# Kernel optimization log

Measured on AMD Instinct MI355X. Metric: run time of the kernel, lower is better.

Reference implementation:

```python
import jax, jax.numpy as jnp
import numpy as np

N_HEADS = 24
ROPE_BASE = 10000.0


def apply_rope(x, offset):
    """x: (B, H, L, Dh). Rotate pairs per RoPE (Su et al., 2021)."""
    B, H, L, Dh = x.shape
    inv_freq = 1.0 / (ROPE_BASE ** (jnp.arange(0, Dh, 2, dtype=jnp.float32) / Dh))  # (Dh/2,)
    t = jnp.arange(L, dtype=jnp.float32) + offset                                   # (L,)
    freqs = jnp.outer(t, inv_freq)                                                  # (L, Dh/2)
    emb = jnp.concatenate([freqs, freqs], axis=-1)                                  # (L, Dh)
    cos = jnp.cos(emb).astype(x.dtype)
    sin = jnp.sin(emb).astype(x.dtype)
    x1, x2 = x[..., : Dh // 2], x[..., Dh // 2 :]
    rotated = jnp.concatenate([-x2, x1], axis=-1)
    return x * cos + rotated * sin


def setup_inputs() -> dict:
    key = jax.random.key(0)
    k1, k2, k3 = jax.random.split(key, 3)
    B, L, D = 4, 2048, 1536
    x = jax.random.normal(k1, (B, L, D), dtype=jnp.float32)
    # Linear weights, torch convention (out_features, in_features), scaled init
    w_qkv = jax.random.normal(k2, (3 * D, D), dtype=jnp.float32) * 0.02
    w_out = jax.random.normal(k3, (D, D), dtype=jnp.float32) * 0.02
    return {"x": x, "w_qkv": w_qkv, "w_out": w_out, "pos_offset": 0}


def reference(x, w_qkv, w_out, pos_offset):
    B, L, D = x.shape
    H = N_HEADS
    Dh = D // H
    # fused QKV projection (no bias)
    qkv = jnp.einsum('bld,ed->ble', x, w_qkv)              # (B, L, 3D)
    qkv = qkv.reshape(B, L, 3, H, Dh)
    q = qkv[:, :, 0].transpose(0, 2, 1, 3)                 # (B, H, L, Dh)
    k = qkv[:, :, 1].transpose(0, 2, 1, 3)
    v = qkv[:, :, 2].transpose(0, 2, 1, 3)
    q = apply_rope(q, pos_offset)
    k = apply_rope(k, pos_offset)
    scale = 1.0 / np.sqrt(Dh)
    scores = jnp.einsum('bhqd,bhkd->bhqk', q, k) * scale   # (B, H, L, L)
    causal = jnp.tril(jnp.ones((L, L), dtype=bool))
    scores = jnp.where(causal, scores, jnp.finfo(scores.dtype).min)
    attn = jax.nn.softmax(scores, axis=-1)
    out = jnp.einsum('bhqk,bhkd->bhqd', attn, v)           # (B, H, L, Dh)
    out = out.transpose(0, 2, 1, 3).reshape(B, L, D)
    return jnp.einsum('bld,ed->ble', out, w_out)           # (B, L, D)
```

## Files before the change

kernel.cpp:

```cpp
#include <hip/hip_runtime.h>
#include <hip/hip_bf16.h>
#include <math.h>

typedef unsigned short u16;
typedef __bf16 b8 __attribute__((ext_vector_type(8)));
typedef __bf16 bf2t __attribute__((ext_vector_type(2)));
typedef float f4 __attribute__((ext_vector_type(4)));

#define B_ 4
#define L_ 2048
#define D_ 1536
#define H_ 24
#define DH_ 64

__device__ __forceinline__ float bf2f(u16 v) {
    union { unsigned u; float f; } z; z.u = ((unsigned)v) << 16; return z.f;
}
__device__ __forceinline__ u16 f2bf(float f) {
    union { float f; unsigned u; } z; z.f = f;
    unsigned u = z.u;
    return (u16)((u + 0x7fffu + ((u >> 16) & 1u)) >> 16);
}
__device__ __forceinline__ void f4_to_bf4(f4 v, u16 o[4]) {
#if __has_builtin(__builtin_amdgcn_cvt_pk_bf16_f32)
    union { bf2t b; unsigned u; } z0, z1;
    z0.b = __builtin_amdgcn_cvt_pk_bf16_f32(v[0], v[1]);
    z1.b = __builtin_amdgcn_cvt_pk_bf16_f32(v[2], v[3]);
    o[0] = (u16)(z0.u & 0xffffu); o[1] = (u16)(z0.u >> 16);
    o[2] = (u16)(z1.u & 0xffffu); o[3] = (u16)(z1.u >> 16);
#else
    o[0] = f2bf(v[0]); o[1] = f2bf(v[1]); o[2] = f2bf(v[2]); o[3] = f2bf(v[3]);
#endif
}

__global__ __launch_bounds__(256) void cvt_f32_bf16(const float* __restrict__ src,
                                                    u16* __restrict__ dst, int n4) {
    int i = blockIdx.x * 256 + threadIdx.x;
    if (i >= n4) return;
    float4 vv = ((const float4*)src)[i];
    f4 v = {vv.x, vv.y, vv.z, vv.w};
    u16 o4[4];
    f4_to_bf4(v, o4);
    ushort4 o = {o4[0], o4[1], o4[2], o4[3]};
    ((ushort4*)dst)[i] = o;
}

__global__ __launch_bounds__(256) void gemm128(const u16* __restrict__ A,
                                               const u16* __restrict__ B,
                                               float* __restrict__ Cf,
                                               u16* __restrict__ Qp,
                                               u16* __restrict__ Kp,
                                               u16* __restrict__ Vp,
                                               int M, int N, int K, int mode) {
    __shared__ u16 As[128 * 32];
    __shared__ u16 Bs[128 * 32];
    const int tid = threadIdx.x;
    const int wave = tid >> 6, lane = tid & 63;
    const int m16 = lane & 15, quad = lane >> 4;
    const int bm = blockIdx.y * 128, bn = blockIdx.x * 128;
    const int wr = (wave >> 1) * 64, wc = (wave & 1) * 64;

    f4 acc[4][4];
#pragma unroll
    for (int i = 0; i < 4; i++)
#pragma unroll
        for (int j = 0; j < 4; j++) acc[i][j] = (f4)0.0f;

    const int c0 = wave * 64 + lane;
    const int r0 = c0 >> 2, col0 = (c0 & 3) * 8;
    const int c1 = c0 + 256;
    const int r1 = c1 >> 2, col1 = (c1 & 3) * 8;

    for (int k0 = 0; k0 < K; k0 += 32) {
        __syncthreads();
        __builtin_amdgcn_global_load_lds(
            (const __attribute__((address_space(1))) void*)(A + (size_t)(bm + r0) * K + k0 + col0),
            (__attribute__((address_space(3))) void*)(As + (size_t)c0 * 8), 16, 0, 0);
        __builtin_amdgcn_global_load_lds(
            (const __attribute__((address_space(1))) void*)(A + (size_t)(bm + r1) * K + k0 + col1),
            (__attribute__((address_space(3))) void*)(As + (size_t)c1 * 8), 16, 0, 0);
        __builtin_amdgcn_global_load_lds(
            (const __attribute__((address_space(1))) void*)(B + (size_t)(bn + r0) * K + k0 + col0),
            (__attribute__((address_space(3))) void*)(Bs + (size_t)c0 * 8), 16, 0, 0);
        __builtin_amdgcn_global_load_lds(
            (const __attribute__((address_space(1))) void*)(B + (size_t)(bn + r1) * K + k0 + col1),
            (__attribute__((address_space(3))) void*)(Bs + (size_t)c1 * 8), 16, 0, 0);
        __syncthreads();
        b8 af[4], bfm[4];
#pragma unroll
        for (int i = 0; i < 4; i++) af[i] = *(const b8*)(As + (wr + i * 16 + m16) * 32 + quad * 8);
#pragma unroll
        for (int j = 0; j < 4; j++) bfm[j] = *(const b8*)(Bs + (wc + j * 16 + m16) * 32 + quad * 8);
#pragma unroll
        for (int i = 0; i < 4; i++)
#pragma unroll
            for (int j = 0; j < 4; j++)
                acc[i][j] = __builtin_amdgcn_mfma_f32_16x16x32_bf16(af[i], bfm[j], acc[i][j], 0, 0, 0);
    }

    if (mode == 0) {
#pragma unroll
        for (int i = 0; i < 4; i++)
#pragma unroll
            for (int j = 0; j < 4; j++)
#pragma unroll
                for (int r = 0; r < 4; r++) {
                    int row = bm + wr + i * 16 + quad * 4 + r;
                    int col = bn + wc + j * 16 + m16;
                    Cf[(size_t)row * N + col] = acc[i][j][r];
                }
    } else {
#pragma unroll
        for (int j = 0; j < 4; j++) {
            const int colbase = bn + wc + j * 16;
            const int s = colbase / D_;
            const int h = (colbase % D_) / DH_;
            const int dh0 = colbase % DH_;
            u16* dst = (s == 0) ? Qp : ((s == 1) ? Kp : Vp);
#pragma unroll
            for (int i = 0; i < 4; i++) {
                u16 o4[4];
                f4_to_bf4(acc[i][j], o4);
#pragma unroll
                for (int r = 0; r < 4; r++) {
                    int row = bm + wr + i * 16 + quad * 4 + r;
                    int b = row >> 11, l = row & (L_ - 1);
                    dst[((size_t)(b * H_ + h) * L_ + l) * DH_ + dh0 + m16] = o4[r];
                }
            }
        }
    }
}

__global__ __launch_bounds__(256) void rope_inplace(u16* __restrict__ Qp,
                                                    u16* __restrict__ Kp,
                                                    const int* __restrict__ pos) {
    unsigned idx = blockIdx.x * 256 + threadIdx.x;
    int i = idx & 31;
    unsigned t1 = idx >> 5;
    int l = t1 & (L_ - 1);
    unsigned t2 = t1 >> 11;
    int h = t2 % H_;
    int b = t2 / H_;
    float t = (float)(l + pos[0]);
    float invf = powf(10000.0f, -(float)(2 * i) * (1.0f / 64.0f));
    float ang = t * invf;
    float c = cosf(ang), s = sinf(ang);
    size_t base = ((size_t)(b * H_ + h) * L_ + l) * DH_;
    {
        float x1 = bf2f(Qp[base + i]), x2 = bf2f(Qp[base + i + 32]);
        Qp[base + i] = f2bf((x1 * c - x2 * s) * 0.125f);
        Qp[base + i + 32] = f2bf((x2 * c + x1 * s) * 0.125f);
    }
    {
        float x1 = bf2f(Kp[base + i]), x2 = bf2f(Kp[base + i + 32]);
        Kp[base + i] = f2bf(x1 * c - x2 * s);
        Kp[base + i + 32] = f2bf(x2 * c + x1 * s);
    }
}

__global__ __launch_bounds__(256, 3) void attn(const u16* __restrict__ Q,
                                               const u16* __restrict__ K,
                                               const u16* __restrict__ V,
                                               u16* __restrict__ O) {
    __shared__ u16 Ks[64 * 72];
    __shared__ u16 Vs[64 * 72];
    __shared__ u16 Ps[4][32 * 72];
    const int tid = threadIdx.x;
    const int wave = tid >> 6, lane = tid & 63;
    const int m16 = lane & 15, quad = lane >> 4;
    const int bh = blockIdx.y;
    const int tA = blockIdx.x;
    const int tB = 15 - tA;
    const int qA = tA * 128 + wave * 32;
    const int qB = tB * 128 + wave * 32;
    const int srow = tid >> 2, scol = (tid & 3) * 16, g = (tid & 3);

    b8 qfA[2][2], qfB[2][2];
#pragma unroll
    for (int i = 0; i < 2; i++) {
        const u16* qa = Q + ((size_t)bh * L_ + qA + i * 16 + m16) * DH_;
        qfA[i][0] = *(const b8*)(qa + quad * 8);
        qfA[i][1] = *(const b8*)(qa + 32 + quad * 8);
        const u16* qb = Q + ((size_t)bh * L_ + qB + i * 16 + m16) * DH_;
        qfB[i][0] = *(const b8*)(qb + quad * 8);
        qfB[i][1] = *(const b8*)(qb + 32 + quad * 8);
    }

    float lrA[2][4], lrB[2][4];
    f4 oaccA[2][4], oaccB[2][4];
#pragma unroll
    for (int i = 0; i < 2; i++)
#pragma unroll
        for (int r = 0; r < 4; r++) { lrA[i][r] = 0.0f; lrB[i][r] = 0.0f; }
#pragma unroll
    for (int i = 0; i < 2; i++)
#pragma unroll
        for (int n = 0; n < 4; n++) { oaccA[i][n] = (f4)0.0f; oaccB[i][n] = (f4)0.0f; }

    u16* pw = Ps[wave];

    auto process = [&](int qw, b8 (&qf)[2][2], float (&lrow)[2][4], f4 (&oacc)[2][4],
                       int kbase) {
        const bool need_mask = (kbase + 64 > qw);
        f4 s[2][4];
#pragma unroll
        for (int sub = 0; sub < 4; sub++) {
            b8 k0 = *(const b8*)(Ks + (sub * 16 + m16) * 72 + quad * 8);
            b8 k1 = *(const b8*)(Ks + (sub * 16 + m16) * 72 + 32 + quad * 8);
#pragma unroll
            for (int i = 0; i < 2; i++) {
                f4 c = (f4)0.0f;
                c = __builtin_amdgcn_mfma_f32_16x16x32_bf16(qf[i][0], k0, c, 0, 0, 0);
                c = __builtin_amdgcn_mfma_f32_16x16x32_bf16(qf[i][1], k1, c, 0, 0, 0);
                s[i][sub] = c;
            }
        }
        if (need_mask) {
#pragma unroll
            for (int i = 0; i < 2; i++)
#pragma unroll
                for (int sub = 0; sub < 4; sub++)
#pragma unroll
                    for (int r = 0; r < 4; r++) {
                        const int key = kbase + sub * 16 + m16;
                        const int qg = qw + i * 16 + quad * 4 + r;
                        float p = __expf(s[i][sub][r]);
                        p = (key <= qg) ? p : 0.0f;
                        s[i][sub][r] = p;
                        lrow[i][r] += p;
                    }
        } else {
#pragma unroll
            for (int i = 0; i < 2; i++)
#pragma unroll
                for (int sub = 0; sub < 4; sub++)
#pragma unroll
                    for (int r = 0; r < 4; r++) {
                        float p = __expf(s[i][sub][r]);
                        s[i][sub][r] = p;
                        lrow[i][r] += p;
                    }
        }
#pragma unroll
        for (int i = 0; i < 2; i++)
#pragma unroll
            for (int sub = 0; sub < 4; sub++) {
                u16 o4[4];
                f4_to_bf4(s[i][sub], o4);
#pragma unroll
                for (int r = 0; r < 4; r++)
                    pw[(i * 16 + quad * 4 + r) * 72 + sub * 16 + m16] = o4[r];
            }
#pragma unroll
        for (int ks = 0; ks < 2; ks++) {
            b8 pf[2];
#pragma unroll
            for (int i = 0; i < 2; i++)
                pf[i] = *(const b8*)(pw + (i * 16 + m16) * 72 + ks * 32 + quad * 8);
#pragma unroll
            for (int n = 0; n < 4; n++) {
                b8 vf = *(const b8*)(Vs + (n * 16 + m16) * 72 +
                                     ((ks * 32 + quad * 8 + n * 16) & 63));
#pragma unroll
                for (int i = 0; i < 2; i++)
                    oacc[i][n] = __builtin_amdgcn_mfma_f32_16x16x32_bf16(pf[i], vf, oacc[i][n], 0, 0, 0);
            }
        }
    };

    const int nkt = 2 * tB + 2;
    for (int kt = 0; kt < nkt; kt++) {
        const int kbase = kt * 64;
        __syncthreads();
        {
            const u16* kg = K + ((size_t)bh * L_ + kbase + srow) * DH_ + scol;
            uint4 a0 = *(const uint4*)kg;
            uint4 a1 = *(const uint4*)(kg + 8);
            const u16* vg = V + ((size_t)bh * L_ + kbase + srow) * DH_ + scol;
            uint4 b0 = *(const uint4*)vg;
            uint4 b1 = *(const uint4*)(vg + 8);
            *(uint4*)(Ks + srow * 72 + scol) = a0;
            *(uint4*)(Ks + srow * 72 + scol + 8) = a1;
            u16 tmp[16];
            *(uint4*)(tmp) = b0;
            *(uint4*)(tmp + 8) = b1;
#pragma unroll
            for (int e = 0; e < 16; e++)
                Vs[(scol + e) * 72 + ((srow + g * 16) & 63)] = tmp[e];
        }
        __syncthreads();
        if (kbase <= qA + 31) process(qA, qfA, lrA, oaccA, kbase);
        if (kbase <= qB + 31) process(qB, qfB, lrB, oaccB, kbase);
    }

#pragma unroll
    for (int x = 1; x < 16; x <<= 1)
#pragma unroll
        for (int i = 0; i < 2; i++)
#pragma unroll
            for (int r = 0; r < 4; r++) {
                lrA[i][r] += __shfl_xor(lrA[i][r], x, 64);
                lrB[i][r] += __shfl_xor(lrB[i][r], x, 64);
            }
    const int b = bh / H_, h = bh % H_;
#pragma unroll
    for (int i = 0; i < 2; i++)
#pragma unroll
        for (int r = 0; r < 4; r++) {
            const float invA = 1.0f / lrA[i][r];
            const float invB = 1.0f / lrB[i][r];
            const int qa = qA + i * 16 + quad * 4 + r;
            const int qb = qB + i * 16 + quad * 4 + r;
#pragma unroll
            for (int n = 0; n < 4; n++) {
                O[((size_t)(b * L_ + qa)) * D_ + h * 64 + n * 16 + m16] = f2bf(oaccA[i][n][r] * invA);
                O[((size_t)(b * L_ + qb)) * D_ + h * 64 + n * 16 + m16] = f2bf(oaccB[i][n][r] * invB);
            }
        }
}

extern "C" void kernel_launch(void* const* d_in, const int* in_sizes, int n_in,
                              void* d_out, int out_size, void* d_ws, size_t ws_size,
                              hipStream_t stream) {
    const float* x = (const float*)d_in[0];
    const float* w_qkv = (const float*)d_in[1];
    const float* w_out = (const float*)d_in[2];
    const int* pos = (const int*)d_in[3];
    float* out = (float*)d_out;

    const size_t nx = (size_t)B_ * L_ * D_;
    const size_t nwq = (size_t)3 * D_ * D_;
    const size_t nwo = (size_t)D_ * D_;
    const size_t per = (size_t)B_ * H_ * L_ * DH_;

    u16* xb = (u16*)d_ws;
    u16* wqkvb = xb + nx;
    u16* woutb = wqkvb + nwq;
    u16* Qp = woutb + nwo;
    u16* Kp = Qp + per;
    u16* Vp = Kp + per;
    u16* aO = xb;

    cvt_f32_bf16<<<(int)((nx / 4 + 255) / 256), 256, 0, stream>>>(x, xb, (int)(nx / 4));
    cvt_f32_bf16<<<(int)((nwq / 4 + 255) / 256), 256, 0, stream>>>(w_qkv, wqkvb, (int)(nwq / 4));
    cvt_f32_bf16<<<(int)((nwo / 4 + 255) / 256), 256, 0, stream>>>(w_out, woutb, (int)(nwo / 4));

    gemm128<<<dim3(3 * D_ / 128, B_ * L_ / 128), 256, 0, stream>>>(
        xb, wqkvb, nullptr, Qp, Kp, Vp, B_ * L_, 3 * D_, D_, 1);
    rope_inplace<<<(B_ * H_ * L_ * 32) / 256, 256, 0, stream>>>(Qp, Kp, pos);
    attn<<<dim3(L_ / 256, B_ * H_), 256, 0, stream>>>(Qp, Kp, Vp, aO);
    gemm128<<<dim3(D_ / 128, B_ * L_ / 128), 256, 0, stream>>>(
        aO, woutb, out, nullptr, nullptr, nullptr, B_ * L_, D_, D_, 0);
}
```

Measured before the change: 522.9 us.

## Replace 128x128 GEMM with double-buffered 256x256 ping-pong pipelined GEMM

Swaps the simple 128x128 tile GEMM, which has one barrier-separated load and compute phase per K=32 step, for a 256x256 tile kernel with 512 threads. It double-buffers K=64 slabs in 128KB of LDS with an XOR-swizzled layout and streams global-to-LDS loads in halves, interleaved with MFMA phases using s_setprio and explicit vmcnt waits. The goal is to hide memory latency behind MFMA work and raise data reuse in both projection GEMMs. The cost is many more barriers, heavy register use, and a smaller grid (e.g. 6x32 blocks for the output projection), which may underfill the CUs.

After: 503.6 us. 3.7% less time.

```diff
diff --git a/kernel.cpp b/kernel.cpp
--- a/kernel.cpp
+++ b/kernel.cpp
@@ -45,87 +45,192 @@
     ((ushort4*)dst)[i] = o;
 }
 
-__global__ __launch_bounds__(256) void gemm128(const u16* __restrict__ A,
-                                               const u16* __restrict__ B,
-                                               float* __restrict__ Cf,
-                                               u16* __restrict__ Qp,
-                                               u16* __restrict__ Kp,
-                                               u16* __restrict__ Vp,
-                                               int M, int N, int K, int mode) {
-    __shared__ u16 As[128 * 32];
-    __shared__ u16 Bs[128 * 32];
+
+__device__ __forceinline__ void stage_half(const u16* __restrict__ G, int Kd,
+                                           int row0, int k0, char* region, int tid) {
+#pragma unroll
+    for (int q = 0; q < 2; q++) {
+        const int p = (q * 512 + tid) * 16;
+        const int l = p ^ (((p >> 9) & 1) << 5);
+        const int grow = row0 + (l >> 11) * 16 + ((l >> 6) & 15);
+        const int gcol = k0 + (((((l >> 10) & 1) << 6) + (l & 63)) >> 1);
+        __builtin_amdgcn_global_load_lds(
+            (const __attribute__((address_space(1))) void*)(G + (size_t)grow * Kd + gcol),
+            (__attribute__((address_space(3))) void*)(region + p), 16, 0, 0);
+    }
+}
+
+template <int BUF, int MH>
+__device__ __forceinline__ void lda(const char* ldsb, int wm, int lo, b8 (&aR)[4][2]) {
+#pragma unroll
+    for (int i = 0; i < 4; i++)
+#pragma unroll
+        for (int ks = 0; ks < 2; ks++)
+            aR[i][ks] = *(const b8*)(ldsb + BUF * 32768 + wm * 16384 +
+                                     ((MH * 4 + i) * 2 + ks) * 1024 + lo);
+}
+template <int BUF, int NH>
+__device__ __forceinline__ void ldb(const char* ldsb, int wn, int lo, b8 (&bR)[4][2]) {
+#pragma unroll
+    for (int j = 0; j < 2; j++)
+#pragma unroll
+        for (int ks = 0; ks < 2; ks++)
+            bR[NH * 2 + j][ks] = *(const b8*)(ldsb + 65536 + BUF * 32768 + (wn >> 1) * 16384 +
+                                              (((wn & 1) * 4 + NH * 2 + j) * 2 + ks) * 1024 + lo);
+}
+template <int MH, int NH>
+__device__ __forceinline__ void mfma16(b8 (&aR)[4][2], b8 (&bR)[4][2], f4 (&acc)[8][4]) {
+    __builtin_amdgcn_s_setprio(1);
+#pragma unroll
+    for (int ks = 0; ks < 2; ks++)
+#pragma unroll
+        for (int i = 0; i < 4; i++)
+#pragma unroll
+            for (int j = 0; j < 2; j++)
+                acc[MH * 4 + i][NH * 2 + j] = __builtin_amdgcn_mfma_f32_16x16x32_bf16(
+                    aR[i][ks], bR[NH * 2 + j][ks], acc[MH * 4 + i][NH * 2 + j], 0, 0, 0);
+    __builtin_amdgcn_s_setprio(0);
+}
+
+__global__ __launch_bounds__(512, 2) void gemm256(const u16* __restrict__ A,
+                                                  const u16* __restrict__ B,
+                                                  float* __restrict__ Cf,
+                                                  u16* __restrict__ Qp,
+                                                  u16* __restrict__ Kp,
+                                                  u16* __restrict__ Vp,
+                                                  int M, int N, int K, int mode) {
+    __shared__ uint4 ldsv[131072 / 16];
+    char* ldsb = (char*)ldsv;
     const int tid = threadIdx.x;
     const int wave = tid >> 6, lane = tid & 63;
     const int m16 = lane & 15, quad = lane >> 4;
-    const int bm = blockIdx.y * 128, bn = blockIdx.x * 128;
-    const int wr = (wave >> 1) * 64, wc = (wave & 1) * 64;
-
-    f4 acc[4][4];
-#pragma unroll
-    for (int i = 0; i < 4; i++)
+    const int wm = wave >> 2, wn = wave & 3;
+    const int bm = blockIdx.y * 256, bn = blockIdx.x * 256;
+    int lo = m16 * 64 + quad * 16;
+    lo ^= (m16 & 8) << 2;
+
+    char* const As0 = ldsb;
+    char* const As1 = ldsb + 32768;
+    char* const Bs0 = ldsb + 65536;
+    char* const Bs1 = ldsb + 98304;
+
+    f4 acc[8][4];
+#pragma unroll
+    for (int i = 0; i < 8; i++)
 #pragma unroll
         for (int j = 0; j < 4; j++) acc[i][j] = (f4)0.0f;
 
-    const int c0 = wave * 64 + lane;
-    const int r0 = c0 >> 2, col0 = (c0 & 3) * 8;
-    const int c1 = c0 + 256;
-    const int r1 = c1 >> 2, col1 = (c1 & 3) * 8;
-
-    for (int k0 = 0; k0 < K; k0 += 32) {
-        __syncthreads();
-        __builtin_amdgcn_global_load_lds(
-            (const __attribute__((address_space(1))) void*)(A + (size_t)(bm + r0) * K + k0 + col0),
-            (__attribute__((address_space(3))) void*)(As + (size_t)c0 * 8), 16, 0, 0);
-        __builtin_amdgcn_global_load_lds(
-            (const __attribute__((address_space(1))) void*)(A + (size_t)(bm + r1) * K + k0 + col1),
-            (__attribute__((address_space(3))) void*)(As + (size_t)c1 * 8), 16, 0, 0);
-        __builtin_amdgcn_global_load_lds(
-            (const __attribute__((address_space(1))) void*)(B + (size_t)(bn + r0) * K + k0 + col0),
-            (__attribute__((address_space(3))) void*)(Bs + (size_t)c0 * 8), 16, 0, 0);
-        __builtin_amdgcn_global_load_lds(
-            (const __attribute__((address_space(1))) void*)(B + (size_t)(bn + r1) * K + k0 + col1),
-            (__attribute__((address_space(3))) void*)(Bs + (size_t)c1 * 8), 16, 0, 0);
-        __syncthreads();
-        b8 af[4], bfm[4];
-#pragma unroll
-        for (int i = 0; i < 4; i++) af[i] = *(const b8*)(As + (wr + i * 16 + m16) * 32 + quad * 8);
-#pragma unroll
-        for (int j = 0; j < 4; j++) bfm[j] = *(const b8*)(Bs + (wc + j * 16 + m16) * 32 + quad * 8);
-#pragma unroll
-        for (int i = 0; i < 4; i++)
-#pragma unroll
-            for (int j = 0; j < 4; j++)
-                acc[i][j] = __builtin_amdgcn_mfma_f32_16x16x32_bf16(af[i], bfm[j], acc[i][j], 0, 0, 0);
+    b8 aR[4][2], bR[4][2];
+
+    stage_half(A, K, bm, 0, As0, tid);
+    stage_half(A, K, bm + 128, 0, As0 + 16384, tid);
+    stage_half(B, K, bn, 0, Bs0, tid);
+    stage_half(B, K, bn + 128, 0, Bs0 + 16384, tid);
+    stage_half(B, K, bn, 64, Bs1, tid);
+    stage_half(A, K, bm, 64, As1, tid);
+    asm volatile("s_waitcnt vmcnt(4)" ::: "memory");
+    __builtin_amdgcn_s_barrier();
+    __builtin_amdgcn_sched_barrier(0);
+
+    const int NIT = K >> 7;
+#pragma unroll 1
+    for (int it = 0; it < NIT; ++it) {
+        const bool more = (it + 1 < NIT);
+        const int k1 = (2 * it + 1) << 6;
+        const int k2 = (2 * it + 2) << 6;
+        const int k3 = (2 * it + 3) << 6;
+
+        lda<0, 0>(ldsb, wm, lo, aR);
+        ldb<0, 0>(ldsb, wn, lo, bR);
+        stage_half(A, K, bm + 128, k1, As1 + 16384, tid);
+        __builtin_amdgcn_s_barrier();
+        mfma16<0, 0>(aR, bR, acc);
+        __builtin_amdgcn_s_barrier();
+
+        ldb<0, 1>(ldsb, wn, lo, bR);
+        stage_half(B, K, bn + 128, k1, Bs1 + 16384, tid);
+        __builtin_amdgcn_s_barrier();
+        mfma16<0, 1>(aR, bR, acc);
+        __builtin_amdgcn_s_barrier();
+
+        lda<0, 1>(ldsb, wm, lo, aR);
+        if (more) stage_half(B, K, bn, k2, Bs0, tid);
+        __builtin_amdgcn_s_barrier();
+        mfma16<1, 0>(aR, bR, acc);
+        __builtin_amdgcn_s_barrier();
+
+        if (more) {
+            stage_half(B, K, bn + 128, k2, Bs0 + 16384, tid);
+            asm volatile("s_waitcnt vmcnt(4)" ::: "memory");
+        } else {
+            asm volatile("s_waitcnt vmcnt(0)" ::: "memory");
+        }
+        __builtin_amdgcn_s_barrier();
+        __builtin_amdgcn_sched_barrier(0);
+        mfma16<1, 1>(aR, bR, acc);
+        __builtin_amdgcn_s_barrier();
+
+        lda<1, 0>(ldsb, wm, lo, aR);
+        ldb<1, 0>(ldsb, wn, lo, bR);
+        if (more) stage_half(A, K, bm, k2, As0, tid);
+        __builtin_amdgcn_s_barrier();
+        mfma16<0, 0>(aR, bR, acc);
+        __builtin_amdgcn_s_barrier();
+
+        ldb<1, 1>(ldsb, wn, lo, bR);
+        if (more) stage_half(A, K, bm + 128, k2, As0 + 16384, tid);
+        __builtin_amdgcn_s_barrier();
+        mfma16<0, 1>(aR, bR, acc);
+        __builtin_amdgcn_s_barrier();
+
+        lda<1, 1>(ldsb, wm, lo, aR);
+        if (more) stage_half(B, K, bn, k3, Bs1, tid);
+        __builtin_amdgcn_s_barrier();
+        mfma16<1, 0>(aR, bR, acc);
+        __builtin_amdgcn_s_barrier();
+
+        if (more) {
+            stage_half(A, K, bm, k3, As1, tid);
+            asm volatile("s_waitcnt vmcnt(4)" ::: "memory");
+        } else {
+            asm volatile("s_waitcnt vmcnt(0)" ::: "memory");
+        }
+        __builtin_amdgcn_s_barrier();
+        __builtin_amdgcn_sched_barrier(0);
+        mfma16<1, 1>(aR, bR, acc);
+        __builtin_amdgcn_s_barrier();
     }
 
     if (mode == 0) {
 #pragma unroll
-        for (int i = 0; i < 4; i++)
-#pragma unroll
-            for (int j = 0; j < 4; j++)
-#pragma unroll
-                for (int r = 0; r < 4; r++) {
-                    int row = bm + wr + i * 16 + quad * 4 + r;
-                    int col = bn + wc + j * 16 + m16;
-                    Cf[(size_t)row * N + col] = acc[i][j][r];
-                }
+        for (int i = 0; i < 8; i++) {
+            const int row = bm + wm * 128 + i * 16 + quad * 4;
+#pragma unroll
+            for (int j = 0; j < 4; j++) {
+                const int col = bn + wn * 64 + j * 16 + m16;
+#pragma unroll
+                for (int r = 0; r < 4; r++)
+                    Cf[(size_t)(row + r) * N + col] = acc[i][j][r];
+            }
+        }
     } else {
 #pragma unroll
         for (int j = 0; j < 4; j++) {
-            const int colbase = bn + wc + j * 16;
+            const int colbase = bn + wn * 64 + j * 16;
             const int s = colbase / D_;
             const int h = (colbase % D_) / DH_;
-            const int dh0 = colbase % DH_;
+            const int dh0 = (colbase % DH_) + m16;
             u16* dst = (s == 0) ? Qp : ((s == 1) ? Kp : Vp);
 #pragma unroll
-            for (int i = 0; i < 4; i++) {
+            for (int i = 0; i < 8; i++) {
                 u16 o4[4];
                 f4_to_bf4(acc[i][j], o4);
+                const int row = bm + wm * 128 + i * 16 + quad * 4;
 #pragma unroll
                 for (int r = 0; r < 4; r++) {
-                    int row = bm + wr + i * 16 + quad * 4 + r;
-                    int b = row >> 11, l = row & (L_ - 1);
-                    dst[((size_t)(b * H_ + h) * L_ + l) * DH_ + dh0 + m16] = o4[r];
+                    const int rr = row + r;
+                    const int b = rr >> 11, l = rr & (L_ - 1);
+                    dst[((size_t)(b * H_ + h) * L_ + l) * DH_ + dh0] = o4[r];
                 }
             }
         }
@@ -346,10 +451,10 @@
     cvt_f32_bf16<<<(int)((nwq / 4 + 255) / 256), 256, 0, stream>>>(w_qkv, wqkvb, (int)(nwq / 4));
     cvt_f32_bf16<<<(int)((nwo / 4 + 255) / 256), 256, 0, stream>>>(w_out, woutb, (int)(nwo / 4));
 
-    gemm128<<<dim3(3 * D_ / 128, B_ * L_ / 128), 256, 0, stream>>>(
+    gemm256<<<dim3(3 * D_ / 256, B_ * L_ / 256), 512, 0, stream>>>(
         xb, wqkvb, nullptr, Qp, Kp, Vp, B_ * L_, 3 * D_, D_, 1);
     rope_inplace<<<(B_ * H_ * L_ * 32) / 256, 256, 0, stream>>>(Qp, Kp, pos);
     attn<<<dim3(L_ / 256, B_ * H_), 256, 0, stream>>>(Qp, Kp, Vp, aO);
-    gemm128<<<dim3(D_ / 128, B_ * L_ / 128), 256, 0, stream>>>(
+    gemm256<<<dim3(D_ / 256, B_ * L_ / 256), 512, 0, stream>>>(
         aO, woutb, out, nullptr, nullptr, nullptr, B_ * L_, D_, D_, 0);
 }
```
